# Kernel tuning notes

Measured on AMD Instinct MI355X. Metric: run time of the kernel, lower is better.

## Reference

```python
import jax, jax.numpy as jnp
import numpy as np

GROUP_SIZE = 64
M, K, N, RANK = 4096, 4096, 4096, 32


def setup_inputs() -> dict:
    key = jax.random.key(0)
    ks = jax.random.split(key, 7)
    x = jax.random.normal(ks[0], (M, K), dtype=jnp.float32)
    # int4 weight residual in [-8, 7]
    q_w = jax.random.randint(ks[1], (K, N), -8, 8, dtype=jnp.int32)
    # positive per-group weight scales, shape (K // group_size, N)
    wscales = jax.random.uniform(ks[2], (K // GROUP_SIZE, N), dtype=jnp.float32) * 0.01 + 1e-4
    lora_down = jax.random.normal(ks[3], (K, RANK), dtype=jnp.float32) * 0.02
    lora_up = jax.random.normal(ks[4], (RANK, N), dtype=jnp.float32) * 0.02
    # smoothing factors, strictly positive
    smooth = jax.random.uniform(ks[5], (K,), dtype=jnp.float32) + 0.5
    bias = jax.random.normal(ks[6], (N,), dtype=jnp.float32)
    return {"x": x, "q_w": q_w, "wscales": wscales, "lora_down": lora_down,
            "lora_up": lora_up, "smooth": smooth, "bias": bias}


def reference(x, q_w, wscales, lora_down, lora_up, smooth, bias):
    G = GROUP_SIZE
    m, k = x.shape
    n = q_w.shape[1]
    ng = k // G  # groups along K

    # smooth activation: move outliers into weights
    x_smooth = x / smooth[None, :]

    # per-group symmetric int4 quantize + dequantize of activations
    xg = x_smooth.reshape(m, ng, G)
    ascales = jnp.maximum(jnp.max(jnp.abs(xg), axis=-1) / 7.0, 1e-8)  # (m, ng)
    qx = jnp.clip(jnp.round(xg / ascales[..., None]), -8.0, 7.0)
    x_dq = (qx * ascales[..., None]).reshape(m, k)

    # dequantize int4 weight residual: grouped along K
    W_dq = (q_w.astype(jnp.float32).reshape(ng, G, n) * wscales[:, None, :]).reshape(k, n)

    # simulated int4 GEMM + fp LoRA residual + bias
    y_main = x_dq @ W_dq
    y_lora = (x @ lora_down) @ lora_up
    return y_main + y_lora + bias[None, :]
```

## Files before the change

### kernel.cpp

```cpp
#include <hip/hip_runtime.h>
#include <hip/hip_bf16.h>
#include <stdint.h>

#define GSIZE 64
#define MDIM 4096
#define KDIM 4096
#define NDIM 4096
#define RANK 32
#define KE   4160
#define NG   64
#define NSPLIT 8

typedef __bf16 bf16x4 __attribute__((ext_vector_type(4)));
typedef __bf16 bf16x8 __attribute__((ext_vector_type(8)));
typedef float  f32x4  __attribute__((ext_vector_type(4)));

#define GPTR(p) ((__attribute__((address_space(1))) void*)(uintptr_t)(p))
#define LPTR(p) ((__attribute__((address_space(3))) void*)(p))

__global__ __launch_bounds__(256) void k_quant(const float* __restrict__ x,
                                               const float* __restrict__ smooth,
                                               __bf16* __restrict__ A,
                                               __bf16* __restrict__ xb) {
    int row = blockIdx.x;
    int tid = threadIdx.x;
    const float4* xr4 = (const float4*)(x + (size_t)row * KDIM);
    const float4* sm4 = (const float4*)smooth;
    __bf16* ar  = A  + (size_t)row * KE;
    __bf16* xbr = xb + (size_t)row * KDIM;
    #pragma unroll
    for (int p = 0; p < 4; ++p) {
        int i4 = p * 256 + tid;
        float4 xv = xr4[i4];
        float4 sv = sm4[i4];
        bf16x4 xbv = {(__bf16)xv.x, (__bf16)xv.y, (__bf16)xv.z, (__bf16)xv.w};
        *(bf16x4*)(xbr + i4 * 4) = xbv;
        float4 xs = {xv.x / sv.x, xv.y / sv.y, xv.z / sv.z, xv.w / sv.w};
        float a = fmaxf(fmaxf(fabsf(xs.x), fabsf(xs.y)),
                        fmaxf(fabsf(xs.z), fabsf(xs.w)));
        #pragma unroll
        for (int off = 1; off < 16; off <<= 1)
            a = fmaxf(a, __shfl_xor(a, off, 64));
        float ascale = fmaxf(a * (1.0f / 7.0f), 1e-8f);
        float q0 = fminf(fmaxf(rintf(xs.x / ascale), -8.f), 7.f);
        float q1 = fminf(fmaxf(rintf(xs.y / ascale), -8.f), 7.f);
        float q2 = fminf(fmaxf(rintf(xs.z / ascale), -8.f), 7.f);
        float q3 = fminf(fmaxf(rintf(xs.w / ascale), -8.f), 7.f);
        bf16x4 av = {(__bf16)(q0 * ascale), (__bf16)(q1 * ascale),
                     (__bf16)(q2 * ascale), (__bf16)(q3 * ascale)};
        *(bf16x4*)(ar + i4 * 4) = av;
    }
}

__global__ __launch_bounds__(256) void k_wprep(const int*   __restrict__ qw,
                                               const float* __restrict__ wsc,
                                               const float* __restrict__ lu,
                                               __bf16* __restrict__ Wt) {
    __shared__ __bf16 tile[64][68];
    int tid = threadIdx.x;
    int n0 = blockIdx.x * 64;
    int kt = blockIdx.y;
    int k0 = kt * 64;
    int tr = tid >> 4;
    int tc = (tid & 15) * 4;
    if (kt < NG) {
        float4 ws = *(const float4*)(wsc + (size_t)kt * NDIM + n0 + tc);
        #pragma unroll
        for (int r = tr; r < 64; r += 16) {
            int4 q = *(const int4*)(qw + (size_t)(k0 + r) * NDIM + n0 + tc);
            tile[r][tc + 0] = (__bf16)((float)q.x * ws.x);
            tile[r][tc + 1] = (__bf16)((float)q.y * ws.y);
            tile[r][tc + 2] = (__bf16)((float)q.z * ws.z);
            tile[r][tc + 3] = (__bf16)((float)q.w * ws.w);
        }
    } else {
        #pragma unroll
        for (int r = tr; r < 64; r += 16) {
            if (r < RANK) {
                float4 lv = *(const float4*)(lu + (size_t)r * NDIM + n0 + tc);
                tile[r][tc + 0] = (__bf16)lv.x;
                tile[r][tc + 1] = (__bf16)lv.y;
                tile[r][tc + 2] = (__bf16)lv.z;
                tile[r][tc + 3] = (__bf16)lv.w;
            } else {
                tile[r][tc + 0] = (__bf16)0.f;
                tile[r][tc + 1] = (__bf16)0.f;
                tile[r][tc + 2] = (__bf16)0.f;
                tile[r][tc + 3] = (__bf16)0.f;
            }
        }
    }
    __syncthreads();
    int nn = tid >> 3;
    int ks = (tid & 7) * 8;
    #pragma unroll
    for (int p = 0; p < 2; ++p) {
        int n = nn + p * 32;
        bf16x8 v;
        #pragma unroll
        for (int e = 0; e < 8; ++e) v[e] = tile[ks + e][n];
        *(bf16x8*)(Wt + (size_t)(n0 + n) * KE + k0 + ks) = v;
    }
}

__global__ __launch_bounds__(256) void k_lorat(const __bf16* __restrict__ xb,
                                               const float*  __restrict__ ld,
                                               float* __restrict__ tws) {
    __shared__ __attribute__((aligned(16))) __bf16 AsL[128 * 32];
    __shared__ __attribute__((aligned(16))) __bf16 BsL[32 * 32];
    int tid  = threadIdx.x;
    int lane = tid & 63;
    int wave = tid >> 6;
    int quad = lane >> 4;
    int mrow = lane & 15;
    int m0    = blockIdx.x * 128;
    int kbase = blockIdx.y * 512;

    f32x4 z = {0.f, 0.f, 0.f, 0.f};
    f32x4 acc[2][2];
    acc[0][0] = z; acc[0][1] = z; acc[1][0] = z; acc[1][1] = z;

    for (int step = 0; step < 16; ++step) {
        int kk = kbase + step * 32;
        const __bf16* Xb = xb + (size_t)m0 * KDIM + kk;
        #pragma unroll
        for (int it = 0; it < 2; ++it) {
            int c = it * 256 + tid;
            int r = c >> 2, kc = (c & 3) * 8;
            int ldsoff = (it * 256 + wave * 64) * 16;
            __builtin_amdgcn_global_load_lds(GPTR(Xb + (size_t)r * KDIM + kc),
                                             LPTR((char*)AsL + ldsoff), 16, 0, 0);
        }
        #pragma unroll
        for (int i2 = 0; i2 < 4; ++i2) {
            int idx = i2 * 256 + tid;
            int r = idx >> 5, n = idx & 31;
            BsL[n * 32 + r] = (__bf16)ld[(size_t)(kk + r) * RANK + n];
        }
        __syncthreads();
        bf16x8 av[2], bv[2];
        #pragma unroll
        for (int i = 0; i < 2; ++i)
            av[i] = *(const bf16x8*)(AsL + (wave * 32 + i * 16 + mrow) * 32 + quad * 8);
        #pragma unroll
        for (int j = 0; j < 2; ++j)
            bv[j] = *(const bf16x8*)(BsL + (j * 16 + mrow) * 32 + quad * 8);
        #pragma unroll
        for (int i = 0; i < 2; ++i)
            #pragma unroll
            for (int j = 0; j < 2; ++j)
                acc[i][j] = __builtin_amdgcn_mfma_f32_16x16x32_bf16(av[i], bv[j], acc[i][j], 0, 0, 0);
        __syncthreads();
    }
    float* tout = tws + (size_t)blockIdx.y * MDIM * RANK;
    #pragma unroll
    for (int i = 0; i < 2; ++i)
        #pragma unroll
        for (int j = 0; j < 2; ++j)
            #pragma unroll
            for (int r = 0; r < 4; ++r) {
                int rowg = m0 + wave * 32 + i * 16 + quad * 4 + r;
                int col  = j * 16 + mrow;
                tout[(size_t)rowg * RANK + col] = acc[i][j][r];
            }
}

__global__ __launch_bounds__(256) void k_fin(const float* __restrict__ tws,
                                             __bf16* __restrict__ A) {
    int idx = blockIdx.x * 256 + threadIdx.x;
    int m = idx >> 6, c = idx & 63;
    float s = 0.f;
    if (c < RANK) {
        #pragma unroll
        for (int sp = 0; sp < NSPLIT; ++sp)
            s += tws[((size_t)sp * MDIM + m) * RANK + c];
    }
    A[(size_t)m * KE + KDIM + c] = (c < RANK) ? (__bf16)s : (__bf16)0.0f;
}

__global__ __launch_bounds__(256) void k_gemm(const __bf16* __restrict__ A,
                                              const __bf16* __restrict__ Wt,
                                              const float*  __restrict__ bias,
                                              float* __restrict__ out) {
    __shared__ __attribute__((aligned(16))) __bf16 As[128 * 64];
    __shared__ __attribute__((aligned(16))) __bf16 Bs[128 * 64];
    int tid  = threadIdx.x;
    int lane = tid & 63;
    int wave = tid >> 6;
    int quad = lane >> 4;
    int mrow = lane & 15;
    int wm = wave >> 1, wn = wave & 1;
    int m0 = blockIdx.y * 128, n0 = blockIdx.x * 128;

    f32x4 z = {0.f, 0.f, 0.f, 0.f};
    f32x4 acc[4][4];
    #pragma unroll
    for (int i = 0; i < 4; ++i)
        #pragma unroll
        for (int j = 0; j < 4; ++j) acc[i][j] = z;

    const __bf16* Ab = A  + (size_t)m0 * KE;
    const __bf16* Bb = Wt + (size_t)n0 * KE;

    for (int kt = 0; kt < KE / 64; ++kt) {
        int k0 = kt * 64;
        #pragma unroll
        for (int it = 0; it < 4; ++it) {
            int c = it * 256 + tid;
            int r = c >> 3;
            int g = (c & 7) ^ (r & 7);
            int ldsoff = (it * 256 + wave * 64) * 16;
            __builtin_amdgcn_global_load_lds(GPTR(Ab + (size_t)r * KE + k0 + g * 8),
                                             LPTR((char*)As + ldsoff), 16, 0, 0);
            __builtin_amdgcn_global_load_lds(GPTR(Bb + (size_t)r * KE + k0 + g * 8),
                                             LPTR((char*)Bs + ldsoff), 16, 0, 0);
        }
        __syncthreads();
        #pragma unroll
        for (int s = 0; s < 2; ++s) {
            bf16x8 av[4], bv[4];
            #pragma unroll
            for (int i = 0; i < 4; ++i) {
                int row  = wm * 64 + i * 16 + mrow;
                int slot = row * 8 + ((s * 4 + quad) ^ (row & 7));
                av[i] = *(const bf16x8*)(As + slot * 8);
            }
            #pragma unroll
            for (int j = 0; j < 4; ++j) {
                int row  = wn * 64 + j * 16 + mrow;
                int slot = row * 8 + ((s * 4 + quad) ^ (row & 7));
                bv[j] = *(const bf16x8*)(Bs + slot * 8);
            }
            #pragma unroll
            for (int i = 0; i < 4; ++i)
                #pragma unroll
                for (int j = 0; j < 4; ++j)
                    acc[i][j] = __builtin_amdgcn_mfma_f32_16x16x32_bf16(av[i], bv[j], acc[i][j], 0, 0, 0);
        }
        __syncthreads();
    }

    #pragma unroll
    for (int j = 0; j < 4; ++j) {
        int col = n0 + wn * 64 + j * 16 + mrow;
        float bvs = bias[col];
        #pragma unroll
        for (int i = 0; i < 4; ++i) {
            int rbase = m0 + wm * 64 + i * 16 + quad * 4;
            #pragma unroll
            for (int r = 0; r < 4; ++r)
                out[(size_t)(rbase + r) * NDIM + col] = acc[i][j][r] + bvs;
        }
    }
}

extern "C" void kernel_launch(void* const* d_in, const int* in_sizes, int n_in,
                              void* d_out, int out_size, void* d_ws, size_t ws_size,
                              hipStream_t stream) {
    const float* x    = (const float*)d_in[0];
    const int*   qw   = (const int*)  d_in[1];
    const float* wsc  = (const float*)d_in[2];
    const float* ld   = (const float*)d_in[3];
    const float* lu   = (const float*)d_in[4];
    const float* sm   = (const float*)d_in[5];
    const float* bias = (const float*)d_in[6];
    float* out = (float*)d_out;

    char* ws = (char*)d_ws;
    __bf16* A   = (__bf16*)ws;
    __bf16* Wt  = (__bf16*)(ws + (size_t)MDIM * KE * 2);
    __bf16* xb  = (__bf16*)(ws + (size_t)MDIM * KE * 4);
    float*  tws = (float*) (ws + (size_t)MDIM * KE * 4
                               + (size_t)MDIM * KDIM * 2);

    k_quant<<<MDIM, 256, 0, stream>>>(x, sm, A, xb);
    k_wprep<<<dim3(NDIM / 64, KE / 64), 256, 0, stream>>>(qw, wsc, lu, Wt);
    k_lorat<<<dim3(MDIM / 128, NSPLIT), 256, 0, stream>>>(xb, ld, tws);
    k_fin<<<(MDIM * 64) / 256, 256, 0, stream>>>(tws, A);
    k_gemm<<<dim3(NDIM / 128, MDIM / 128), 256, 0, stream>>>(A, Wt, bias, out);
}
```

Baseline: 375.0 us.

## Merge quant, weight prep and LoRA-down into one launch; drop bf16 x copy

After: 352.0 us. 1.07x faster.

```diff
diff --git a/kernel.cpp b/kernel.cpp
--- a/kernel.cpp
+++ b/kernel.cpp
@@ -11,6 +11,10 @@
 #define NG   64
 #define NSPLIT 8
 
+#define B_QUANT 4096
+#define B_WPREP (B_QUANT + 65 * 64)
+#define B_LORAT (B_WPREP + 32 * NSPLIT)
+
 typedef __bf16 bf16x4 __attribute__((ext_vector_type(4)));
 typedef __bf16 bf16x8 __attribute__((ext_vector_type(8)));
 typedef float  f32x4  __attribute__((ext_vector_type(4)));
@@ -18,164 +22,184 @@
 #define GPTR(p) ((__attribute__((address_space(1))) void*)(uintptr_t)(p))
 #define LPTR(p) ((__attribute__((address_space(3))) void*)(p))
 
-__global__ __launch_bounds__(256) void k_quant(const float* __restrict__ x,
-                                               const float* __restrict__ smooth,
-                                               __bf16* __restrict__ A,
-                                               __bf16* __restrict__ xb) {
-    int row = blockIdx.x;
+__global__ __launch_bounds__(256) void k_prep(const float* __restrict__ x,
+                                              const int*   __restrict__ qw,
+                                              const float* __restrict__ wsc,
+                                              const float* __restrict__ ld,
+                                              const float* __restrict__ lu,
+                                              const float* __restrict__ smooth,
+                                              __bf16* __restrict__ A,
+                                              __bf16* __restrict__ Wt,
+                                              float* __restrict__ tws) {
+    __shared__ __attribute__((aligned(16))) char smem[10240];
+    int b   = blockIdx.x;
     int tid = threadIdx.x;
-    const float4* xr4 = (const float4*)(x + (size_t)row * KDIM);
-    const float4* sm4 = (const float4*)smooth;
-    __bf16* ar  = A  + (size_t)row * KE;
-    __bf16* xbr = xb + (size_t)row * KDIM;
-    #pragma unroll
-    for (int p = 0; p < 4; ++p) {
-        int i4 = p * 256 + tid;
-        float4 xv = xr4[i4];
-        float4 sv = sm4[i4];
-        bf16x4 xbv = {(__bf16)xv.x, (__bf16)xv.y, (__bf16)xv.z, (__bf16)xv.w};
-        *(bf16x4*)(xbr + i4 * 4) = xbv;
-        float4 xs = {xv.x / sv.x, xv.y / sv.y, xv.z / sv.z, xv.w / sv.w};
-        float a = fmaxf(fmaxf(fabsf(xs.x), fabsf(xs.y)),
-                        fmaxf(fabsf(xs.z), fabsf(xs.w)));
-        #pragma unroll
-        for (int off = 1; off < 16; off <<= 1)
-            a = fmaxf(a, __shfl_xor(a, off, 64));
-        float ascale = fmaxf(a * (1.0f / 7.0f), 1e-8f);
-        float q0 = fminf(fmaxf(rintf(xs.x / ascale), -8.f), 7.f);
-        float q1 = fminf(fmaxf(rintf(xs.y / ascale), -8.f), 7.f);
-        float q2 = fminf(fmaxf(rintf(xs.z / ascale), -8.f), 7.f);
-        float q3 = fminf(fmaxf(rintf(xs.w / ascale), -8.f), 7.f);
-        bf16x4 av = {(__bf16)(q0 * ascale), (__bf16)(q1 * ascale),
-                     (__bf16)(q2 * ascale), (__bf16)(q3 * ascale)};
-        *(bf16x4*)(ar + i4 * 4) = av;
-    }
-}
-
-__global__ __launch_bounds__(256) void k_wprep(const int*   __restrict__ qw,
-                                               const float* __restrict__ wsc,
-                                               const float* __restrict__ lu,
-                                               __bf16* __restrict__ Wt) {
-    __shared__ __bf16 tile[64][68];
-    int tid = threadIdx.x;
-    int n0 = blockIdx.x * 64;
-    int kt = blockIdx.y;
-    int k0 = kt * 64;
-    int tr = tid >> 4;
-    int tc = (tid & 15) * 4;
-    if (kt < NG) {
-        float4 ws = *(const float4*)(wsc + (size_t)kt * NDIM + n0 + tc);
-        #pragma unroll
-        for (int r = tr; r < 64; r += 16) {
-            int4 q = *(const int4*)(qw + (size_t)(k0 + r) * NDIM + n0 + tc);
-            tile[r][tc + 0] = (__bf16)((float)q.x * ws.x);
-            tile[r][tc + 1] = (__bf16)((float)q.y * ws.y);
-            tile[r][tc + 2] = (__bf16)((float)q.z * ws.z);
-            tile[r][tc + 3] = (__bf16)((float)q.w * ws.w);
-        }
-    } else {
-        #pragma unroll
-        for (int r = tr; r < 64; r += 16) {
-            if (r < RANK) {
-                float4 lv = *(const float4*)(lu + (size_t)r * NDIM + n0 + tc);
-                tile[r][tc + 0] = (__bf16)lv.x;
-                tile[r][tc + 1] = (__bf16)lv.y;
-                tile[r][tc + 2] = (__bf16)lv.z;
-                tile[r][tc + 3] = (__bf16)lv.w;
-            } else {
-                tile[r][tc + 0] = (__bf16)0.f;
-                tile[r][tc + 1] = (__bf16)0.f;
-                tile[r][tc + 2] = (__bf16)0.f;
-                tile[r][tc + 3] = (__bf16)0.f;
-            }
-        }
-    }
-    __syncthreads();
-    int nn = tid >> 3;
-    int ks = (tid & 7) * 8;
-    #pragma unroll
-    for (int p = 0; p < 2; ++p) {
-        int n = nn + p * 32;
-        bf16x8 v;
-        #pragma unroll
-        for (int e = 0; e < 8; ++e) v[e] = tile[ks + e][n];
-        *(bf16x8*)(Wt + (size_t)(n0 + n) * KE + k0 + ks) = v;
-    }
-}
-
-__global__ __launch_bounds__(256) void k_lorat(const __bf16* __restrict__ xb,
-                                               const float*  __restrict__ ld,
-                                               float* __restrict__ tws) {
-    __shared__ __attribute__((aligned(16))) __bf16 AsL[128 * 32];
-    __shared__ __attribute__((aligned(16))) __bf16 BsL[32 * 32];
-    int tid  = threadIdx.x;
-    int lane = tid & 63;
-    int wave = tid >> 6;
-    int quad = lane >> 4;
-    int mrow = lane & 15;
-    int m0    = blockIdx.x * 128;
-    int kbase = blockIdx.y * 512;
-
-    f32x4 z = {0.f, 0.f, 0.f, 0.f};
-    f32x4 acc[2][2];
-    acc[0][0] = z; acc[0][1] = z; acc[1][0] = z; acc[1][1] = z;
-
-    for (int step = 0; step < 16; ++step) {
-        int kk = kbase + step * 32;
-        const __bf16* Xb = xb + (size_t)m0 * KDIM + kk;
-        #pragma unroll
-        for (int it = 0; it < 2; ++it) {
-            int c = it * 256 + tid;
-            int r = c >> 2, kc = (c & 3) * 8;
-            int ldsoff = (it * 256 + wave * 64) * 16;
-            __builtin_amdgcn_global_load_lds(GPTR(Xb + (size_t)r * KDIM + kc),
-                                             LPTR((char*)AsL + ldsoff), 16, 0, 0);
-        }
-        #pragma unroll
-        for (int i2 = 0; i2 < 4; ++i2) {
-            int idx = i2 * 256 + tid;
-            int r = idx >> 5, n = idx & 31;
-            BsL[n * 32 + r] = (__bf16)ld[(size_t)(kk + r) * RANK + n];
+
+    if (b < B_QUANT) {
+        int row = b;
+        const float4* xr4 = (const float4*)(x + (size_t)row * KDIM);
+        const float4* sm4 = (const float4*)smooth;
+        __bf16* ar = A + (size_t)row * KE;
+        #pragma unroll
+        for (int p = 0; p < 4; ++p) {
+            int i4 = p * 256 + tid;
+            float4 xv = xr4[i4];
+            float4 sv = sm4[i4];
+            float4 xs = {xv.x * __builtin_amdgcn_rcpf(sv.x),
+                         xv.y * __builtin_amdgcn_rcpf(sv.y),
+                         xv.z * __builtin_amdgcn_rcpf(sv.z),
+                         xv.w * __builtin_amdgcn_rcpf(sv.w)};
+            float a = fmaxf(fmaxf(fabsf(xs.x), fabsf(xs.y)),
+                            fmaxf(fabsf(xs.z), fabsf(xs.w)));
+            #pragma unroll
+            for (int off = 1; off < 16; off <<= 1)
+                a = fmaxf(a, __shfl_xor(a, off, 64));
+            float ascale = fmaxf(a * (1.0f / 7.0f), 1e-8f);
+            float rin = __builtin_amdgcn_rcpf(ascale);
+            float q0 = fminf(fmaxf(rintf(xs.x * rin), -8.f), 7.f);
+            float q1 = fminf(fmaxf(rintf(xs.y * rin), -8.f), 7.f);
+            float q2 = fminf(fmaxf(rintf(xs.z * rin), -8.f), 7.f);
+            float q3 = fminf(fmaxf(rintf(xs.w * rin), -8.f), 7.f);
+            bf16x4 av = {(__bf16)(q0 * ascale), (__bf16)(q1 * ascale),
+                         (__bf16)(q2 * ascale), (__bf16)(q3 * ascale)};
+            *(bf16x4*)(ar + i4 * 4) = av;
+        }
+        return;
+    }
+
+    if (b < B_WPREP) {
+        __bf16 (*tile)[68] = (__bf16(*)[68])smem;
+        int idx = b - B_QUANT;
+        int n0 = (idx & 63) * 64;
+        int kt = idx >> 6;
+        int k0 = kt * 64;
+        int tr = tid >> 4;
+        int tc = (tid & 15) * 4;
+        if (kt < NG) {
+            float4 ws = *(const float4*)(wsc + (size_t)kt * NDIM + n0 + tc);
+            #pragma unroll
+            for (int r = tr; r < 64; r += 16) {
+                int4 q = *(const int4*)(qw + (size_t)(k0 + r) * NDIM + n0 + tc);
+                tile[r][tc + 0] = (__bf16)((float)q.x * ws.x);
+                tile[r][tc + 1] = (__bf16)((float)q.y * ws.y);
+                tile[r][tc + 2] = (__bf16)((float)q.z * ws.z);
+                tile[r][tc + 3] = (__bf16)((float)q.w * ws.w);
+            }
+        } else {
+            #pragma unroll
+            for (int r = tr; r < 64; r += 16) {
+                if (r < RANK) {
+                    float4 lv = *(const float4*)(lu + (size_t)r * NDIM + n0 + tc);
+                    tile[r][tc + 0] = (__bf16)lv.x;
+                    tile[r][tc + 1] = (__bf16)lv.y;
+                    tile[r][tc + 2] = (__bf16)lv.z;
+                    tile[r][tc + 3] = (__bf16)lv.w;
+                } else {
+                    tile[r][tc + 0] = (__bf16)0.f;
+                    tile[r][tc + 1] = (__bf16)0.f;
+                    tile[r][tc + 2] = (__bf16)0.f;
+                    tile[r][tc + 3] = (__bf16)0.f;
+                }
+            }
         }
         __syncthreads();
-        bf16x8 av[2], bv[2];
+        int nn = tid >> 3;
+        int ks = (tid & 7) * 8;
+        #pragma unroll
+        for (int p = 0; p < 2; ++p) {
+            int n = nn + p * 32;
+            bf16x8 v;
+            #pragma unroll
+            for (int e = 0; e < 8; ++e) v[e] = tile[ks + e][n];
+            *(bf16x8*)(Wt + (size_t)(n0 + n) * KE + k0 + ks) = v;
+        }
+        return;
+    }
+
+    {
+        __bf16* AsL = (__bf16*)smem;
+        __bf16* BsL = (__bf16*)(smem + 8192);
+        int idx  = b - B_WPREP;
+        int m0    = (idx & 31) * 128;
+        int sp    = idx >> 5;
+        int kbase = sp * 512;
+        int lane = tid & 63;
+        int wave = tid >> 6;
+        int quad = lane >> 4;
+        int mrow = lane & 15;
+
+        f32x4 z = {0.f, 0.f, 0.f, 0.f};
+        f32x4 acc[2][2];
+        acc[0][0] = z; acc[0][1] = z; acc[1][0] = z; acc[1][1] = z;
+
+        for (int step = 0; step < 16; ++step) {
+            int kk = kbase + step * 32;
+            #pragma unroll
+            for (int it = 0; it < 2; ++it) {
+                int slot = it * 256 + tid;
+                int r = slot >> 2;
+                int g = (slot & 3) ^ (r & 3);
+                const float* src = x + (size_t)(m0 + r) * KDIM + kk + g * 8;
+                float4 a0 = *(const float4*)src;
+                float4 a1 = *(const float4*)(src + 4);
+                bf16x8 v = {(__bf16)a0.x, (__bf16)a0.y, (__bf16)a0.z, (__bf16)a0.w,
+                            (__bf16)a1.x, (__bf16)a1.y, (__bf16)a1.z, (__bf16)a1.w};
+                *(bf16x8*)(AsL + slot * 8) = v;
+            }
+            #pragma unroll
+            for (int i2 = 0; i2 < 4; ++i2) {
+                int j = i2 * 256 + tid;
+                int r = j >> 5, n = j & 31;
+                BsL[n * 32 + r] = (__bf16)ld[(size_t)(kk + r) * RANK + n];
+            }
+            __syncthreads();
+            bf16x8 av[2], bv[2];
+            #pragma unroll
+            for (int i = 0; i < 2; ++i) {
+                int row  = wave * 32 + i * 16 + mrow;
+                int slot = row * 4 + (quad ^ (row & 3));
+                av[i] = *(const bf16x8*)(AsL + slot * 8);
+            }
+            #pragma unroll
+            for (int j = 0; j < 2; ++j)
+                bv[j] = *(const bf16x8*)(BsL + (j * 16 + mrow) * 32 + quad * 8);
+            #pragma unroll
+            for (int i = 0; i < 2; ++i)
+                #pragma unroll
+                for (int j = 0; j < 2; ++j)
+                    acc[i][j] = __builtin_amdgcn_mfma_f32_16x16x32_bf16(av[i], bv[j], acc[i][j], 0, 0, 0);
+            __syncthreads();
+        }
+        float* tout = tws + (size_t)sp * MDIM * RANK;
         #pragma unroll
         for (int i = 0; i < 2; ++i)
-            av[i] = *(const bf16x8*)(AsL + (wave * 32 + i * 16 + mrow) * 32 + quad * 8);
-        #pragma unroll
-        for (int j = 0; j < 2; ++j)
-            bv[j] = *(const bf16x8*)(BsL + (j * 16 + mrow) * 32 + quad * 8);
-        #pragma unroll
-        for (int i = 0; i < 2; ++i)
             #pragma unroll
             for (int j = 0; j < 2; ++j)
-                acc[i][j] = __builtin_amdgcn_mfma_f32_16x16x32_bf16(av[i], bv[j], acc[i][j], 0, 0, 0);
-        __syncthreads();
-    }
-    float* tout = tws + (size_t)blockIdx.y * MDIM * RANK;
-    #pragma unroll
-    for (int i = 0; i < 2; ++i)
-        #pragma unroll
-        for (int j = 0; j < 2; ++j)
-            #pragma unroll
-            for (int r = 0; r < 4; ++r) {
-                int rowg = m0 + wave * 32 + i * 16 + quad * 4 + r;
-                int col  = j * 16 + mrow;
-                tout[(size_t)rowg * RANK + col] = acc[i][j][r];
-            }
+                #pragma unroll
+                for (int r = 0; r < 4; ++r) {
+                    int rowg = m0 + wave * 32 + i * 16 + quad * 4 + r;
+                    int col  = j * 16 + mrow;
+                    tout[(size_t)rowg * RANK + col] = acc[i][j][r];
+                }
+    }
 }
 
 __global__ __launch_bounds__(256) void k_fin(const float* __restrict__ tws,
                                              __bf16* __restrict__ A) {
     int idx = blockIdx.x * 256 + threadIdx.x;
-    int m = idx >> 6, c = idx & 63;
-    float s = 0.f;
+    int m = idx >> 4, cq = idx & 15;
+    int c = cq * 4;
+    bf16x4 v = {(__bf16)0.f, (__bf16)0.f, (__bf16)0.f, (__bf16)0.f};
     if (c < RANK) {
-        #pragma unroll
-        for (int sp = 0; sp < NSPLIT; ++sp)
-            s += tws[((size_t)sp * MDIM + m) * RANK + c];
-    }
-    A[(size_t)m * KE + KDIM + c] = (c < RANK) ? (__bf16)s : (__bf16)0.0f;
+        f32x4 s = {0.f, 0.f, 0.f, 0.f};
+        #pragma unroll
+        for (int sp = 0; sp < NSPLIT; ++sp) {
+            f32x4 p = *(const f32x4*)(tws + ((size_t)sp * MDIM + m) * RANK + c);
+            s.x += p.x; s.y += p.y; s.z += p.z; s.w += p.w;
+        }
+        v[0] = (__bf16)s.x; v[1] = (__bf16)s.y; v[2] = (__bf16)s.z; v[3] = (__bf16)s.w;
+    }
+    *(bf16x4*)(A + (size_t)m * KE + KDIM + c) = v;
 }
 
 __global__ __launch_bounds__(256) void k_gemm(const __bf16* __restrict__ A,
@@ -269,13 +293,9 @@
     char* ws = (char*)d_ws;
     __bf16* A   = (__bf16*)ws;
     __bf16* Wt  = (__bf16*)(ws + (size_t)MDIM * KE * 2);
-    __bf16* xb  = (__bf16*)(ws + (size_t)MDIM * KE * 4);
-    float*  tws = (float*) (ws + (size_t)MDIM * KE * 4
-                               + (size_t)MDIM * KDIM * 2);
-
-    k_quant<<<MDIM, 256, 0, stream>>>(x, sm, A, xb);
-    k_wprep<<<dim3(NDIM / 64, KE / 64), 256, 0, stream>>>(qw, wsc, lu, Wt);
-    k_lorat<<<dim3(MDIM / 128, NSPLIT), 256, 0, stream>>>(xb, ld, tws);
-    k_fin<<<(MDIM * 64) / 256, 256, 0, stream>>>(tws, A);
+    float*  tws = (float*) (ws + (size_t)MDIM * KE * 4);
+
+    k_prep<<<B_LORAT, 256, 0, stream>>>(x, qw, wsc, ld, lu, sm, A, Wt, tws);
+    k_fin<<<(MDIM * 16) / 256, 256, 0, stream>>>(tws, A);
     k_gemm<<<dim3(NDIM / 128, MDIM / 128), 256, 0, stream>>>(A, Wt, bias, out);
 }
```
